# Kernel tuning notes

Measured on AMD Instinct MI355X. Metric: run time of the kernel, lower is better.

## Reference

```python
import jax, jax.numpy as jnp
import numpy as np

RANK = 64          # rank
ENT_COMPS = 5      # ent_comps (1 time + 4 space components per rank slot)
REL_COMPS = 4      # rel_comps (quaternion / boost velocity)
N_ENT = 80000
N_REL = 500
B = 2000
INIT_SIZE = 0.001
SCALE = 1.0 / np.sqrt(RANK)
EPS = 1e-9


def _quat_mul(q, p):
    # Hamilton product of quaternions q, p: [..., 4] each, layout (w, x, y, z)
    qw, qx, qy, qz = q[..., 0], q[..., 1], q[..., 2], q[..., 3]
    pw, px, py, pz = p[..., 0], p[..., 1], p[..., 2], p[..., 3]
    return jnp.stack([
        qw * pw - qx * px - qy * py - qz * pz,
        qw * px + qx * pw + qy * pz - qz * py,
        qw * py - qx * pz + qy * pw + qz * px,
        qw * pz + qx * py - qy * px + qz * pw,
    ], axis=-1)


def lorentz_rotate(x, r):
    # x: [B, R, 5] Lorentz vectors (t, s4); r: [B, R, 4] rotation quaternion.
    # Spatial 4D isoclinic rotation via unit-quaternion left multiplication; time fixed.
    q = r * jax.lax.rsqrt(jnp.sum(r * r, axis=-1, keepdims=True) + EPS)
    t, s = x[..., :1], x[..., 1:]
    return jnp.concatenate([t, _quat_mul(q, s)], axis=-1)


def lorentz_boost(x, v):
    # x: [B, R, 5]; v: [B, R, 4] boost velocity (|v| < 1).
    t, s = x[..., :1], x[..., 1:]
    vn2 = jnp.clip(jnp.sum(v * v, axis=-1, keepdims=True), 0.0, 0.999)  # [B,R,1]
    gamma = jax.lax.rsqrt(1.0 - vn2)
    vs = jnp.sum(v * s, axis=-1, keepdims=True)
    t2 = gamma * (t + vs)
    s2 = s + (gamma * t + (gamma - 1.0) * vs / (vn2 + EPS)) * v
    return jnp.concatenate([t2, s2], axis=-1)


def setup_inputs() -> dict:
    key = jax.random.key(0)
    k = jax.random.split(key, 6)
    queries = jax.random.randint(k[0], (B, 3), 0, N_REL, dtype=jnp.int32)
    stru_entities = jax.random.normal(k[1], (N_ENT, 2 * RANK, ENT_COMPS), jnp.float32) * INIT_SIZE
    stru_rel_rotate = jax.random.normal(k[2], (N_REL, RANK, REL_COMPS), jnp.float32) * INIT_SIZE
    stru_rel_boosts = jax.random.normal(k[3], (N_REL, RANK, REL_COMPS), jnp.float32) * INIT_SIZE
    stru_atten = jax.random.normal(k[4], (N_REL, 1, ENT_COMPS * RANK), jnp.float32) * INIT_SIZE
    stru_rel_aux = jax.random.normal(k[5], (N_REL, 2, ENT_COMPS * RANK), jnp.float32) * INIT_SIZE
    return {
        "queries": queries,
        "stru_entities": stru_entities,
        "stru_rel_rotate": stru_rel_rotate,
        "stru_rel_boosts": stru_rel_boosts,
        "stru_atten": stru_atten,
        "stru_rel_aux": stru_rel_aux,
    }


def reference(queries, stru_entities, stru_rel_rotate, stru_rel_boosts, stru_atten, stru_rel_aux):
    b = queries.shape[0]
    D = ENT_COMPS * RANK  # 320
    h, r, t = queries[:, 0], queries[:, 1], queries[:, 2]

    slhs = stru_entities[h]                       # [B, 2R, 5]
    srhs = stru_entities[t]                       # [B, 2R, 5]
    lhs_re = slhs[:, :RANK]                       # [B, R, 5]
    lhs_im = slhs[:, RANK:].reshape(b, D)         # [B, D]
    rhs_re = srhs[:, :RANK].reshape(b, D)
    rhs_im = srhs[:, RANK:].reshape(b, D)

    rrot = stru_rel_rotate[r]                     # [B, R, 4]
    rboost = stru_rel_boosts[r]                   # [B, R, 4]
    atten = stru_atten[r]                         # [B, 1, D]
    aux = stru_rel_aux[r]                         # [B, 2, D]
    aux0, aux1 = aux[:, 0], aux[:, 1]

    to_re = stru_entities[:, :RANK].reshape(N_ENT, D)
    to_im = stru_entities[:, RANK:].reshape(N_ENT, D)

    rot = lorentz_rotate(lhs_re, rrot).reshape(b, D, 1)
    boo = lorentz_boost(lhs_re, rboost).reshape(b, D, 1)
    cands = jnp.concatenate([rot, boo], axis=-1)              # [B, D, 2]
    weights = jax.nn.softmax(jnp.matmul(atten * SCALE, cands), axis=-1)  # [B, 1, 2]
    lhs = jnp.sum(cands * weights, axis=-1)                   # [B, D]

    scores = (lhs * aux0 - lhs_im * aux1) @ to_re.T \
           + (lhs * aux1 + lhs_im * aux0) @ to_im.T           # [B, N_ENT]

    reg0 = jnp.sqrt(lhs_re.reshape(b, D) ** 2 + lhs_im ** 2)
    reg1 = jnp.sqrt(aux0 ** 2 + aux1 ** 2)
    reg2 = jnp.sqrt(rhs_re ** 2 + rhs_im ** 2) * (1.0 / 3.0)
    reg3 = jnp.sqrt(jnp.sum(rrot ** 2, axis=-1))
    reg4 = jnp.sqrt(jnp.sum(rboost ** 2, axis=-1))
    return scores, reg0, reg1, reg2, reg3, reg4
```

## Files before the change

kernel.cpp:

```cpp
#include <hip/hip_runtime.h>
#include <math.h>

#define RANK 64
#define D_DIM 320
#define K_DIM 640
#define N_ENT 80000
#define B_Q 2000
#define M_PAD 2048
#define NBLK_N 313
#define SCALE_F 0.125f
#define EPS_F 1e-9f

#define OFF_SCORES 0ull
#define OFF_REG0 160000000ull
#define OFF_REG1 160640000ull
#define OFF_REG2 161280000ull
#define OFF_REG3 161920000ull
#define OFF_REG4 162048000ull

typedef __attribute__((ext_vector_type(8))) short short8v;
typedef __attribute__((ext_vector_type(4))) float floatx4;

typedef __attribute__((address_space(1))) const unsigned int gu32;
typedef __attribute__((address_space(3))) unsigned int lu32;

static __device__ __forceinline__ unsigned short f2bf(float f) {
    union { float f; unsigned int u; } a; a.f = f;
    unsigned int u = a.u;
    u += 0x7FFFu + ((u >> 16) & 1u);
    return (unsigned short)(u >> 16);
}

__global__ __launch_bounds__(64) void prep_kernel(
    const int* __restrict__ q,
    const float* __restrict__ ent,
    const float* __restrict__ rrot_t,
    const float* __restrict__ rboost_t,
    const float* __restrict__ atten_t,
    const float* __restrict__ aux_t,
    unsigned short* __restrict__ X,
    float* __restrict__ out)
{
    int b = blockIdx.x;
    int lane = threadIdx.x;
    unsigned short* Xrow = X + (size_t)b * K_DIM;

    if (b >= B_Q) {
        #pragma unroll
        for (int c = 0; c < 10; c++) Xrow[lane * 10 + c] = 0;
        return;
    }

    int h = q[3 * b + 0];
    int r = q[3 * b + 1];
    int t = q[3 * b + 2];

    const float* eh = ent + (size_t)h * K_DIM;
    const float* et = ent + (size_t)t * K_DIM;

    float4 rv = *(const float4*)(rrot_t + (size_t)r * 256 + lane * 4);
    float4 bv = *(const float4*)(rboost_t + (size_t)r * 256 + lane * 4);

    const float* xr = eh + lane * 5;
    float x0 = xr[0], x1 = xr[1], x2 = xr[2], x3 = xr[3], x4 = xr[4];

    float rr2 = rv.x * rv.x + rv.y * rv.y + rv.z * rv.z + rv.w * rv.w;
    float rb2 = bv.x * bv.x + bv.y * bv.y + bv.z * bv.z + bv.w * bv.w;

    float qinv = 1.0f / sqrtf(rr2 + EPS_F);
    float qw = rv.x * qinv, qx = rv.y * qinv, qy = rv.z * qinv, qz = rv.w * qinv;
    float pw = x1, px = x2, py = x3, pz = x4;
    float rot[5];
    rot[0] = x0;
    rot[1] = qw * pw - qx * px - qy * py - qz * pz;
    rot[2] = qw * px + qx * pw + qy * pz - qz * py;
    rot[3] = qw * py - qx * pz + qy * pw + qz * px;
    rot[4] = qw * pz + qx * py - qy * px + qz * pw;

    float vn2 = fminf(fmaxf(rb2, 0.0f), 0.999f);
    float sq = sqrtf(1.0f - vn2);
    float gamma = 1.0f / sq;
    float gm1 = vn2 / (sq * (1.0f + sq));
    float vs = bv.x * x1 + bv.y * x2 + bv.z * x3 + bv.w * x4;
    float boo[5];
    boo[0] = gamma * (x0 + vs);
    float coef = gamma * x0 + gm1 * vs / (vn2 + EPS_F);
    boo[1] = x1 + coef * bv.x;
    boo[2] = x2 + coef * bv.y;
    boo[3] = x3 + coef * bv.z;
    boo[4] = x4 + coef * bv.w;

    const float* at = atten_t + (size_t)r * D_DIM + lane * 5;
    float w0 = at[0] * rot[0] + at[1] * rot[1] + at[2] * rot[2] + at[3] * rot[3] + at[4] * rot[4];
    float w1 = at[0] * boo[0] + at[1] * boo[1] + at[2] * boo[2] + at[3] * boo[3] + at[4] * boo[4];
    #pragma unroll
    for (int off = 32; off; off >>= 1) {
        w0 += __shfl_xor(w0, off);
        w1 += __shfl_xor(w1, off);
    }
    w0 *= SCALE_F;
    w1 *= SCALE_F;
    float mx = fmaxf(w0, w1);
    float e0 = expf(w0 - mx), e1 = expf(w1 - mx);
    float inv = 1.0f / (e0 + e1);
    float wt0 = e0 * inv, wt1 = e1 * inv;

    const float* a0p = aux_t + (size_t)r * 640 + lane * 5;
    const float* a1p = a0p + D_DIM;
    float xre[5] = {x0, x1, x2, x3, x4};

    #pragma unroll
    for (int c = 0; c < 5; c++) {
        int d = lane * 5 + c;
        float lhs = wt0 * rot[c] + wt1 * boo[c];
        float im = eh[D_DIM + d];
        float a0 = a0p[c], a1 = a1p[c];
        Xrow[d]         = f2bf(lhs * a0 - im * a1);
        Xrow[D_DIM + d] = f2bf(lhs * a1 + im * a0);
        out[OFF_REG0 + (size_t)b * D_DIM + d] = sqrtf(xre[c] * xre[c] + im * im);
        out[OFF_REG1 + (size_t)b * D_DIM + d] = sqrtf(a0 * a0 + a1 * a1);
        float tre = et[d], tim = et[D_DIM + d];
        out[OFF_REG2 + (size_t)b * D_DIM + d] = sqrtf(tre * tre + tim * tim) * (1.0f / 3.0f);
    }
    out[OFF_REG3 + (size_t)b * RANK + lane] = sqrtf(rr2);
    out[OFF_REG4 + (size_t)b * RANK + lane] = sqrtf(rb2);
}

__global__ __launch_bounds__(256) void convE_kernel(
    const float* __restrict__ Ef, unsigned short* __restrict__ Eb)
{
    const size_t n4 = (size_t)N_ENT * K_DIM / 4;
    size_t stride = (size_t)gridDim.x * blockDim.x;
    for (size_t v = (size_t)blockIdx.x * blockDim.x + threadIdx.x; v < n4; v += stride) {
        float4 f = ((const float4*)Ef)[v];
        ushort4 u;
        u.x = f2bf(f.x); u.y = f2bf(f.y); u.z = f2bf(f.z); u.w = f2bf(f.w);
        ((ushort4*)Eb)[v] = u;
    }
}

__global__ __launch_bounds__(512, 2) void gemm256(
    const unsigned short* __restrict__ X,
    const unsigned short* __restrict__ Eb,
    float* __restrict__ C)
{
    __shared__ unsigned short lds[65536];

    const int tid = threadIdx.x;
    const int lane = tid & 63;
    const int wid = tid >> 6;
    const int wm = wid >> 2;
    const int wn = wid & 3;

    int bid = blockIdx.x;
    int swz = (bid & 7) * NBLK_N + (bid >> 3);
    const int m0 = (swz / NBLK_N) * 256;
    const int n0 = (swz % NBLK_N) * 256;

    const int fr = lane & 15;
    const int kq = lane >> 4;

    floatx4 acc[8][4];
    #pragma unroll
    for (int i = 0; i < 8; i++)
        #pragma unroll
        for (int j = 0; j < 4; j++) acc[i][j] = (floatx4)0.0f;

    const int srow = tid >> 3;
    const int scol_sw = ((tid & 7) ^ ((tid >> 3) & 7)) * 8;
    const int sdst = srow * 64 + (tid & 7) * 8;

    auto stage = [&](int buf, int kt) {
        const int k0 = kt * 64;
        const int Ab = buf * 16384;
        const int Bb = 32768 + buf * 16384;
        #pragma unroll
        for (int r = 0; r < 4; r++) {
            const unsigned short* ga = X + (size_t)(m0 + r * 64 + srow) * K_DIM + k0 + scol_sw;
            __builtin_amdgcn_global_load_lds((gu32*)ga, (lu32*)&lds[Ab + r * 4096 + sdst], 16, 0, 0);
        }
        #pragma unroll
        for (int r = 0; r < 4; r++) {
            int grow = n0 + r * 64 + srow;
            if (grow > N_ENT - 1) grow = N_ENT - 1;
            const unsigned short* gb = Eb + (size_t)grow * K_DIM + k0 + scol_sw;
            __builtin_amdgcn_global_load_lds((gu32*)gb, (lu32*)&lds[Bb + r * 4096 + sdst], 16, 0, 0);
        }
    };

    stage(0, 0);
    __syncthreads();

    int buf = 0;
    for (int kt = 0; kt < K_DIM / 64; kt++) {
        if (kt < K_DIM / 64 - 1) stage(buf ^ 1, kt + 1);

        const int Ab = buf * 16384;
        const int Bb = 32768 + buf * 16384;
        #pragma unroll
        for (int ks = 0; ks < 2; ks++) {
            short8v a[8], b[4];
            const int swk = ((ks * 4 + kq) ^ (fr & 7)) * 8;
            #pragma unroll
            for (int i = 0; i < 8; i++) {
                int row = wm * 128 + i * 16 + fr;
                a[i] = *(const short8v*)&lds[Ab + row * 64 + swk];
            }
            #pragma unroll
            for (int j = 0; j < 4; j++) {
                int row = wn * 64 + j * 16 + fr;
                b[j] = *(const short8v*)&lds[Bb + row * 64 + swk];
            }
            #pragma unroll
            for (int i = 0; i < 8; i++)
                #pragma unroll
                for (int j = 0; j < 4; j++)
                    acc[i][j] = __builtin_amdgcn_mfma_f32_16x16x32_bf16(a[i], b[j], acc[i][j], 0, 0, 0);
        }
        __syncthreads();
        buf ^= 1;
    }

    const int rb = kq * 4;
    #pragma unroll
    for (int i = 0; i < 8; i++) {
        #pragma unroll
        for (int j = 0; j < 4; j++) {
            int row = m0 + wm * 128 + i * 16 + rb;
            int col = n0 + wn * 64 + j * 16 + fr;
            if (col < N_ENT) {
                #pragma unroll
                for (int r = 0; r < 4; r++) {
                    if (row + r < B_Q)
                        C[(size_t)(row + r) * N_ENT + col] = acc[i][j][r];
                }
            }
        }
    }
}

__global__ __launch_bounds__(256) void gemm_mfma_fb(
    const unsigned short* __restrict__ X,
    const float* __restrict__ Ef,
    float* __restrict__ C)
{
    __shared__ unsigned short As[128 * 32];
    __shared__ unsigned short Bs[128 * 32];

    const int tid = threadIdx.x;
    const int lane = tid & 63;
    const int wave = tid >> 6;
    const int wm = wave >> 1, wn = wave & 1;
    const int m0 = blockIdx.x * 128;
    const int n0 = blockIdx.y * 128;

    floatx4 acc[4][4];
    #pragma unroll
    for (int i = 0; i < 4; i++)
        #pragma unroll
        for (int j = 0; j < 4; j++) acc[i][j] = (floatx4)0.0f;

    const int srow = tid >> 2;
    const int scol = (tid & 3) * 8;
    const int fr = lane & 15;
    const int kb = (lane >> 4) * 8;
    const int brow_f = tid >> 1;
    const int bcol_f = (tid & 1) * 16;

    for (int k0 = 0; k0 < K_DIM; k0 += 32) {
        __syncthreads();
        #pragma unroll
        for (int r = 0; r < 2; r++) {
            const unsigned short* gp = X + (size_t)(m0 + srow + r * 64) * K_DIM + k0 + scol;
            __builtin_amdgcn_global_load_lds((gu32*)gp, (lu32*)(As + (size_t)(r * 64 + srow) * 32 + scol), 16, 0, 0);
        }
        {
            const float* ep = Ef + (size_t)(n0 + brow_f) * K_DIM + k0 + bcol_f;
            float4 f0 = *(const float4*)(ep);
            float4 f1 = *(const float4*)(ep + 4);
            float4 f2 = *(const float4*)(ep + 8);
            float4 f3 = *(const float4*)(ep + 12);
            short8v p0, p1;
            p0[0] = (short)f2bf(f0.x); p0[1] = (short)f2bf(f0.y);
            p0[2] = (short)f2bf(f0.z); p0[3] = (short)f2bf(f0.w);
            p0[4] = (short)f2bf(f1.x); p0[5] = (short)f2bf(f1.y);
            p0[6] = (short)f2bf(f1.z); p0[7] = (short)f2bf(f1.w);
            p1[0] = (short)f2bf(f2.x); p1[1] = (short)f2bf(f2.y);
            p1[2] = (short)f2bf(f2.z); p1[3] = (short)f2bf(f2.w);
            p1[4] = (short)f2bf(f3.x); p1[5] = (short)f2bf(f3.y);
            p1[6] = (short)f2bf(f3.z); p1[7] = (short)f2bf(f3.w);
            *(short8v*)(Bs + (size_t)brow_f * 32 + bcol_f) = p0;
            *(short8v*)(Bs + (size_t)brow_f * 32 + bcol_f + 8) = p1;
        }
        __syncthreads();

        short8v a[4], b[4];
        #pragma unroll
        for (int i = 0; i < 4; i++)
            a[i] = *(const short8v*)(As + (size_t)(wm * 64 + i * 16 + fr) * 32 + kb);
        #pragma unroll
        for (int j = 0; j < 4; j++)
            b[j] = *(const short8v*)(Bs + (size_t)(wn * 64 + j * 16 + fr) * 32 + kb);

        #pragma unroll
        for (int i = 0; i < 4; i++)
            #pragma unroll
            for (int j = 0; j < 4; j++)
                acc[i][j] = __builtin_amdgcn_mfma_f32_16x16x32_bf16(a[i], b[j], acc[i][j], 0, 0, 0);
    }

    const int rbase = (lane >> 4) * 4;
    #pragma unroll
    for (int i = 0; i < 4; i++) {
        #pragma unroll
        for (int j = 0; j < 4; j++) {
            int row = m0 + wm * 64 + i * 16 + rbase;
            int col = n0 + wn * 64 + j * 16 + fr;
            #pragma unroll
            for (int r = 0; r < 4; r++) {
                if (row + r < B_Q)
                    C[(size_t)(row + r) * N_ENT + col] = acc[i][j][r];
            }
        }
    }
}

extern "C" void kernel_launch(void* const* d_in, const int* in_sizes, int n_in,
                              void* d_out, int out_size, void* d_ws, size_t ws_size,
                              hipStream_t stream) {
    const int* queries = (const int*)d_in[0];
    const float* ent = (const float*)d_in[1];
    const float* rrot = (const float*)d_in[2];
    const float* rboost = (const float*)d_in[3];
    const float* atten = (const float*)d_in[4];
    const float* aux = (const float*)d_in[5];
    float* out = (float*)d_out;

    unsigned short* X = (unsigned short*)d_ws;
    const size_t offE = (size_t)M_PAD * K_DIM * 2;
    const size_t needE = (size_t)N_ENT * K_DIM * 2;
    unsigned short* Eb = (unsigned short*)((char*)d_ws + offE);
    bool pre = (ws_size >= offE + needE);

    prep_kernel<<<M_PAD, 64, 0, stream>>>(queries, ent, rrot, rboost, atten, aux, X, out);

    if (pre) {
        convE_kernel<<<2048, 256, 0, stream>>>(ent, Eb);
        gemm256<<<8 * NBLK_N, 512, 0, stream>>>(X, Eb, out + OFF_SCORES);
    } else {
        dim3 grid(M_PAD / 128, N_ENT / 128);
        gemm_mfma_fb<<<grid, 256, 0, stream>>>(X, ent, out + OFF_SCORES);
    }
}
```

Before: 389.8 us.

## Restructure bf16 GEMM main loop into fine-grained phased pipeline with explicit waitcnts

Splits each 64-wide K tile into four phases (two k-halves by two M-halves), each issuing a quarter of the next tile's global-to-LDS loads before running 16 MFMAs. Explicit vmcnt/lgkmcnt waits, raw s_barriers, sched_barrier and setprio replace the per-tile __syncthreads, and the LDS layout moves to 32-element k-halves with a new XOR swizzle. Occupancy is lowered to one block per CU and the block-index swizzle is replaced by a plain M-fastest mapping. The goal is to overlap memory latency with MFMA work at the cost of more barriers and hand-tuned wait counts that must match the number of loads in flight.

```diff
diff --git a/kernel.cpp b/kernel.cpp
--- a/kernel.cpp
+++ b/kernel.cpp
@@ -8,6 +8,7 @@
 #define B_Q 2000
 #define M_PAD 2048
 #define NBLK_N 313
+#define NT 10
 #define SCALE_F 0.125f
 #define EPS_F 1e-9f
 
@@ -23,6 +24,11 @@
 
 typedef __attribute__((address_space(1))) const unsigned int gu32;
 typedef __attribute__((address_space(3))) unsigned int lu32;
+
+#define VMCNT6() asm volatile("s_waitcnt vmcnt(6)" ::: "memory")
+#define VMCNT4() asm volatile("s_waitcnt vmcnt(4)" ::: "memory")
+#define VMCNT0() asm volatile("s_waitcnt vmcnt(0)" ::: "memory")
+#define LGKM0()  asm volatile("s_waitcnt lgkmcnt(0)" ::: "memory")
 
 static __device__ __forceinline__ unsigned short f2bf(float f) {
     union { float f; unsigned int u; } a; a.f = f;
@@ -139,7 +145,7 @@
     }
 }
 
-__global__ __launch_bounds__(512, 2) void gemm256(
+__global__ __launch_bounds__(512, 1) void gemm256(
     const unsigned short* __restrict__ X,
     const unsigned short* __restrict__ Eb,
     float* __restrict__ C)
@@ -153,12 +159,12 @@
     const int wn = wid & 3;
 
     int bid = blockIdx.x;
-    int swz = (bid & 7) * NBLK_N + (bid >> 3);
-    const int m0 = (swz / NBLK_N) * 256;
-    const int n0 = (swz % NBLK_N) * 256;
+    const int m0 = (bid & 7) * 256;
+    const int n0 = (bid >> 3) * 256;
 
     const int fr = lane & 15;
     const int kq = lane >> 4;
+    const int cbs8 = (kq ^ ((fr >> 1) & 3)) * 8;
 
     floatx4 acc[8][4];
     #pragma unroll
@@ -166,60 +172,84 @@
         #pragma unroll
         for (int j = 0; j < 4; j++) acc[i][j] = (floatx4)0.0f;
 
-    const int srow = tid >> 3;
-    const int scol_sw = ((tid & 7) ^ ((tid >> 3) & 7)) * 8;
-    const int sdst = srow * 64 + (tid & 7) * 8;
-
-    auto stage = [&](int buf, int kt) {
-        const int k0 = kt * 64;
-        const int Ab = buf * 16384;
-        const int Bb = 32768 + buf * 16384;
-        #pragma unroll
-        for (int r = 0; r < 4; r++) {
-            const unsigned short* ga = X + (size_t)(m0 + r * 64 + srow) * K_DIM + k0 + scol_sw;
-            __builtin_amdgcn_global_load_lds((gu32*)ga, (lu32*)&lds[Ab + r * 4096 + sdst], 16, 0, 0);
-        }
-        #pragma unroll
-        for (int r = 0; r < 4; r++) {
-            int grow = n0 + r * 64 + srow;
-            if (grow > N_ENT - 1) grow = N_ENT - 1;
-            const unsigned short* gb = Eb + (size_t)grow * K_DIM + k0 + scol_sw;
-            __builtin_amdgcn_global_load_lds((gu32*)gb, (lu32*)&lds[Bb + r * 4096 + sdst], 16, 0, 0);
+    const int srow = tid >> 2;
+    const int scb = tid & 3;
+
+    auto stage_ht = [&](int bufOff, int kt, int h) {
+        const int mat = h & 1, kk = h >> 1;
+        const int base = bufOff + mat * 16384 + kk * 8192;
+        #pragma unroll
+        for (int l = 0; l < 2; l++) {
+            int row = srow + l * 128;
+            int colg = kk * 32 + ((scb ^ ((row >> 1) & 3)) * 8);
+            const unsigned short* gp;
+            if (mat == 0) {
+                gp = X + (size_t)(m0 + row) * K_DIM + kt * 64 + colg;
+            } else {
+                int grow = n0 + row;
+                if (grow > N_ENT - 1) grow = N_ENT - 1;
+                gp = Eb + (size_t)grow * K_DIM + kt * 64 + colg;
+            }
+            __builtin_amdgcn_global_load_lds((gu32*)gp,
+                (lu32*)&lds[base + row * 32 + scb * 8], 16, 0, 0);
         }
     };
 
-    stage(0, 0);
-    __syncthreads();
-
-    int buf = 0;
-    for (int kt = 0; kt < K_DIM / 64; kt++) {
-        if (kt < K_DIM / 64 - 1) stage(buf ^ 1, kt + 1);
-
-        const int Ab = buf * 16384;
-        const int Bb = 32768 + buf * 16384;
-        #pragma unroll
-        for (int ks = 0; ks < 2; ks++) {
-            short8v a[8], b[4];
-            const int swk = ((ks * 4 + kq) ^ (fr & 7)) * 8;
-            #pragma unroll
-            for (int i = 0; i < 8; i++) {
-                int row = wm * 128 + i * 16 + fr;
-                a[i] = *(const short8v*)&lds[Ab + row * 64 + swk];
-            }
-            #pragma unroll
-            for (int j = 0; j < 4; j++) {
-                int row = wn * 64 + j * 16 + fr;
-                b[j] = *(const short8v*)&lds[Bb + row * 64 + swk];
-            }
-            #pragma unroll
-            for (int i = 0; i < 8; i++)
-                #pragma unroll
-                for (int j = 0; j < 4; j++)
-                    acc[i][j] = __builtin_amdgcn_mfma_f32_16x16x32_bf16(a[i], b[j], acc[i][j], 0, 0, 0);
-        }
-        __syncthreads();
-        buf ^= 1;
-    }
+#define PHASE(KK, IH, WAITM, PF)                                              \
+    {                                                                         \
+        const unsigned short* Ab_ = lds + bufo + (KK) * 8192;                 \
+        const unsigned short* Bb_ = lds + bufo + 16384 + (KK) * 8192;         \
+        short8v a_[4], b_[4];                                                 \
+        _Pragma("unroll")                                                     \
+        for (int i2 = 0; i2 < 4; i2++) {                                      \
+            int row = wm * 128 + ((IH) * 4 + i2) * 16 + fr;                   \
+            a_[i2] = *(const short8v*)&Ab_[row * 32 + cbs8];                  \
+        }                                                                     \
+        _Pragma("unroll")                                                     \
+        for (int j = 0; j < 4; j++) {                                         \
+            int row = wn * 64 + j * 16 + fr;                                  \
+            b_[j] = *(const short8v*)&Bb_[row * 32 + cbs8];                   \
+        }                                                                     \
+        if (PF) stage_ht(nbo, t + 1, (KK) * 2 + (IH));                        \
+        WAITM();                                                              \
+        __builtin_amdgcn_s_barrier();                                         \
+        LGKM0();                                                              \
+        __builtin_amdgcn_sched_barrier(0);                                    \
+        __builtin_amdgcn_s_setprio(1);                                        \
+        _Pragma("unroll")                                                     \
+        for (int i2 = 0; i2 < 4; i2++)                                        \
+            _Pragma("unroll")                                                 \
+            for (int j = 0; j < 4; j++)                                       \
+                acc[(IH) * 4 + i2][j] = __builtin_amdgcn_mfma_f32_16x16x32_bf16( \
+                    a_[i2], b_[j], acc[(IH) * 4 + i2][j], 0, 0, 0);           \
+        __builtin_amdgcn_s_setprio(0);                                        \
+        __builtin_amdgcn_s_barrier();                                        \
+    }
+
+    #pragma unroll
+    for (int h = 0; h < 4; h++) stage_ht(0, 0, h);
+    VMCNT0();
+    __builtin_amdgcn_s_barrier();
+
+    for (int t = 0; t < NT - 1; t++) {
+        const int bufo = (t & 1) * 32768;
+        const int nbo = bufo ^ 32768;
+        PHASE(0, 0, VMCNT6, true)
+        PHASE(0, 1, VMCNT4, true)
+        PHASE(1, 0, VMCNT6, true)
+        PHASE(1, 1, VMCNT4, true)
+    }
+    {
+        const int t = NT - 1;
+        const int bufo = (t & 1) * 32768;
+        const int nbo = bufo ^ 32768;
+        (void)nbo;
+        PHASE(0, 0, VMCNT4, false)
+        PHASE(0, 1, VMCNT0, false)
+        PHASE(1, 0, VMCNT0, false)
+        PHASE(1, 1, VMCNT0, false)
+    }
+#undef PHASE
 
     const int rb = kq * 4;
     #pragma unroll
```

Result: slower. 403.5 us (+3.5%).
